# Optimization experiments

Measured on AMD Instinct MI355X. Metric: run time of the kernel, lower is better.

The kernel has to match this reference:

```python
import jax, jax.numpy as jnp
import numpy as np
import math

VOCAB = 50257
BLOCK = 2048
NE = 768


def setup_inputs() -> dict:
    key = jax.random.key(0)
    ks = jax.random.split(key, 12)
    s = 0.02
    idx = jax.random.randint(ks[0], (4, 2048), 0, VOCAB, dtype=jnp.int64 if jax.config.jax_enable_x64 else jnp.int32)
    tok_emb = jax.random.normal(ks[1], (VOCAB, NE), jnp.float32) * s
    pos_emb = jax.random.normal(ks[2], (BLOCK, NE), jnp.float32) * s
    Wk = jax.random.normal(ks[3], (NE, NE), jnp.float32) * s
    bk = jnp.zeros((NE,), jnp.float32)
    Wq = jax.random.normal(ks[4], (NE, NE), jnp.float32) * s
    bq = jnp.zeros((NE,), jnp.float32)
    Wv = jax.random.normal(ks[5], (NE, NE), jnp.float32) * s
    bv = jnp.zeros((NE,), jnp.float32)
    ln_g = jnp.ones((NE,), jnp.float32)
    ln_b = jnp.zeros((NE,), jnp.float32)
    Wh = jax.random.normal(ks[6], (NE, VOCAB), jnp.float32) * s
    bh = jnp.zeros((VOCAB,), jnp.float32)
    return {"idx": idx, "tok_emb": tok_emb, "pos_emb": pos_emb, "Wq": Wq, "bq": bq,
            "Wk": Wk, "bk": bk, "Wv": Wv, "bv": bv, "ln_g": ln_g, "ln_b": ln_b,
            "Wh": Wh, "bh": bh}


def reference(idx, tok_emb, pos_emb, Wq, bq, Wk, bk, Wv, bv, ln_g, ln_b, Wh, bh):
    B, T = idx.shape
    C = tok_emb.shape[1]
    x = tok_emb[idx] + pos_emb[:T]  # [B,T,C]
    q = jnp.einsum('btc,cd->btd', x, Wq) + bq
    k = jnp.einsum('btc,cd->btd', x, Wk) + bk
    v = jnp.einsum('btc,cd->btd', x, Wv) + bv
    att = jnp.einsum('btd,bsd->bts', q, k) / math.sqrt(C)  # [B,T,T]
    causal = jnp.tril(jnp.ones((T, T), bool))
    att = jnp.where(causal, att, -jnp.inf)
    att = jax.nn.softmax(att, axis=-1)
    y = jnp.einsum('bts,bsd->btd', att, v)
    # LayerNorm (eps=1e-5, torch default)
    mu = jnp.mean(y, axis=-1, keepdims=True)
    var = jnp.mean((y - mu) ** 2, axis=-1, keepdims=True)
    yn = (y - mu) * jax.lax.rsqrt(var + 1e-5) * ln_g + ln_b
    logits = jnp.einsum('btc,cv->btv', yn, Wh) + bh
    return logits
```

## Files before the change

kernel.cpp:

```cpp
#include <hip/hip_runtime.h>
#include <hip/hip_bf16.h>
#include <math.h>

typedef __bf16 bf16x8 __attribute__((ext_vector_type(8)));
typedef float  f32x4  __attribute__((ext_vector_type(4)));

#define GAS(p) ((const __attribute__((address_space(1))) void*)(p))
#define LAS(p) ((__attribute__((address_space(3))) void*)(p))

static constexpr int NE = 768;

__global__ __launch_bounds__(256) void k_embed(const int* __restrict__ idx,
    const float* __restrict__ tok, const float* __restrict__ pos,
    __hip_bfloat16* __restrict__ xb)
{
    int bt = blockIdx.x;
    int t  = bt & 2047;
    int token = idx[bt];
    const float* te = tok + (size_t)token * NE;
    const float* pe = pos + (size_t)t * NE;
    __hip_bfloat16* o = xb + (size_t)bt * NE;
    for (int c = threadIdx.x; c < NE; c += 256)
        o[c] = __float2bfloat16(te[c] + pe[c]);
}

__global__ __launch_bounds__(256) void k_transpose_f32_bf16(
    const float* __restrict__ in, __hip_bfloat16* __restrict__ out,
    int R, int C, int outRows)
{
    __shared__ float tile[32][33];
    int c0 = blockIdx.x * 32, r0 = blockIdx.y * 32;
    int tx = threadIdx.x & 31, ty = threadIdx.x >> 5;
    #pragma unroll
    for (int i = 0; i < 32; i += 8) {
        int r = r0 + ty + i, c = c0 + tx;
        tile[ty + i][tx] = (r < R && c < C) ? in[(size_t)r * C + c] : 0.f;
    }
    __syncthreads();
    #pragma unroll
    for (int i = 0; i < 32; i += 8) {
        int oc = c0 + ty + i, orr = r0 + tx;
        if (oc < outRows && orr < R)
            out[(size_t)oc * R + orr] = __float2bfloat16(tile[tx][ty + i]);
    }
}

__global__ __launch_bounds__(256) void k_transpose_bf16(
    const __hip_bfloat16* __restrict__ in, __hip_bfloat16* __restrict__ out,
    int R, int C)
{
    __shared__ __hip_bfloat16 tile[32][33];
    size_t boff = (size_t)blockIdx.z * R * C;
    int c0 = blockIdx.x * 32, r0 = blockIdx.y * 32;
    int tx = threadIdx.x & 31, ty = threadIdx.x >> 5;
    #pragma unroll
    for (int i = 0; i < 32; i += 8)
        tile[ty + i][tx] = in[boff + (size_t)(r0 + ty + i) * C + (c0 + tx)];
    __syncthreads();
    #pragma unroll
    for (int i = 0; i < 32; i += 8)
        out[boff + (size_t)(c0 + ty + i) * R + (r0 + tx)] = tile[tx][ty + i];
}

__global__ __launch_bounds__(256) void k_pack_bias(const float* __restrict__ bq,
    const float* __restrict__ bk, const float* __restrict__ bv, float* __restrict__ o)
{
    int i = blockIdx.x * 256 + threadIdx.x;
    if (i < 768) o[i] = bq[i];
    else if (i < 1536) o[i] = bk[i - 768];
    else if (i < 2304) o[i] = bv[i - 1536];
}

template<int MODE>
__global__ __launch_bounds__(256) void k_gemm(
    const __hip_bfloat16* __restrict__ A, const __hip_bfloat16* __restrict__ Bt,
    int K, int lda, int ldb,
    size_t strideA, size_t strideB, size_t strideC,
    float* __restrict__ outf, int ldc, int ncols,
    const float* __restrict__ bias, float scale,
    __hip_bfloat16* __restrict__ oq, __hip_bfloat16* __restrict__ ok,
    __hip_bfloat16* __restrict__ ov)
{
    int bn = blockIdx.x, bm = blockIdx.y, bz = blockIdx.z;
    if (MODE == 1 && bn > bm) return;
    __shared__ __align__(16) __hip_bfloat16 As[128 * 32];
    __shared__ __align__(16) __hip_bfloat16 Bs[128 * 32];
    const __hip_bfloat16* Ab = A  + bz * strideA + (size_t)bm * 128 * lda;
    const __hip_bfloat16* Bb = Bt + bz * strideB + (size_t)bn * 128 * ldb;
    int tid = threadIdx.x, w = tid >> 6, lane = tid & 63;
    int wr = w >> 1, wc = w & 1;
    f32x4 acc[4][4] = {};
    int sr = tid >> 2, sc = (tid & 3) * 8;
    int lr = lane & 15, lk = (lane >> 4) * 8;

    for (int k0 = 0; k0 < K; k0 += 32) {
        __syncthreads();
        #pragma unroll
        for (int i = 0; i < 2; ++i) {
            __builtin_amdgcn_global_load_lds(GAS(Ab + (size_t)(i * 64 + sr) * lda + k0 + sc),
                                             LAS((char*)As + i * 4096 + w * 1024), 16, 0, 0);
            __builtin_amdgcn_global_load_lds(GAS(Bb + (size_t)(i * 64 + sr) * ldb + k0 + sc),
                                             LAS((char*)Bs + i * 4096 + w * 1024), 16, 0, 0);
        }
        __syncthreads();
        bf16x8 af[4], bfv[4];
        #pragma unroll
        for (int mi = 0; mi < 4; ++mi)
            af[mi] = *(const bf16x8*)(As + (wr * 64 + mi * 16 + lr) * 32 + lk);
        #pragma unroll
        for (int ni = 0; ni < 4; ++ni)
            bfv[ni] = *(const bf16x8*)(Bs + (wc * 64 + ni * 16 + lr) * 32 + lk);
        #pragma unroll
        for (int mi = 0; mi < 4; ++mi)
            #pragma unroll
            for (int ni = 0; ni < 4; ++ni)
                acc[mi][ni] = __builtin_amdgcn_mfma_f32_16x16x32_bf16(af[mi], bfv[ni], acc[mi][ni], 0, 0, 0);
    }

    int r4 = (lane >> 4) * 4;
    #pragma unroll
    for (int mi = 0; mi < 4; ++mi) {
        #pragma unroll
        for (int ni = 0; ni < 4; ++ni) {
            #pragma unroll
            for (int r = 0; r < 4; ++r) {
                int row = bm * 128 + wr * 64 + mi * 16 + r4 + r;
                int col = bn * 128 + wc * 64 + ni * 16 + lr;
                float v = acc[mi][ni][r];
                if constexpr (MODE == 0) {
                    v += bias[col];
                    __hip_bfloat16 h = __float2bfloat16(v);
                    if (col < 768)       oq[(size_t)row * 768 + col]          = h;
                    else if (col < 1536) ok[(size_t)row * 768 + (col - 768)]  = h;
                    else                 ov[(size_t)row * 768 + (col - 1536)] = h;
                } else if constexpr (MODE == 1) {
                    outf[bz * strideC + (size_t)row * ldc + col] = v * scale;
                } else {
                    outf[bz * strideC + (size_t)row * ldc + col] = v;
                }
            }
        }
    }
}

__global__ __launch_bounds__(512, 2) void k_gemm_head(
    const __hip_bfloat16* __restrict__ A,
    const __hip_bfloat16* __restrict__ Bt,
    float* __restrict__ out, const float* __restrict__ bias, int ldc, int ncols)
{
    constexpr int K = 768, NT = K / 64;
    __shared__ __align__(16) __hip_bfloat16 As[2][256 * 64];
    __shared__ __align__(16) __hip_bfloat16 Bs[2][256 * 64];

    const int bn = blockIdx.x, bm = blockIdx.y;
    const int tid = threadIdx.x;
    const int w = tid >> 6, lane = tid & 63;
    const int wr = w >> 2, wc = w & 3;
    const int lr = lane & 15, lu = lane >> 4;
    const int rswz = lr & 7;

    const int srow = tid >> 3;
    const int sunit = (tid & 7) ^ (srow & 7);
    const size_t Abase = (size_t)bm * 256 * K;
    const size_t Bbase = (size_t)bn * 256 * K;

    auto stageA = [&](int kt, int c, int p) {
        const __hip_bfloat16* src = A + Abase + (size_t)(c * 64 + srow) * K + kt * 64 + sunit * 8;
        __builtin_amdgcn_global_load_lds(GAS(src), LAS(&As[p][c * 4096 + tid * 8]), 16, 0, 0);
    };
    auto stageB = [&](int kt, int c, int p) {
        const __hip_bfloat16* src = Bt + Bbase + (size_t)(c * 64 + srow) * K + kt * 64 + sunit * 8;
        __builtin_amdgcn_global_load_lds(GAS(src), LAS(&Bs[p][c * 4096 + tid * 8]), 16, 0, 0);
    };
    auto rdA = [&](int p, int m, int kk) {
        return *(const bf16x8*)&As[p][(wr * 128 + m * 16 + lr) * 64 + ((kk * 4 + lu) ^ rswz) * 8];
    };
    auto rdB = [&](int p, int n, int kk) {
        return *(const bf16x8*)&Bs[p][(wc * 64 + n * 16 + lr) * 64 + ((kk * 4 + lu) ^ rswz) * 8];
    };

    f32x4 acc[8][4] = {};

    stageB(0, 0, 0); stageB(0, 1, 0); stageB(0, 2, 0); stageB(0, 3, 0);
    stageA(0, 0, 0); stageA(0, 1, 0); stageA(0, 2, 0); stageA(0, 3, 0);
    stageB(1, 0, 1); stageB(1, 1, 1); stageB(1, 2, 1); stageB(1, 3, 1);
    stageA(1, 0, 1); stageA(1, 2, 1);

#define QUAD(Q)                                                                                          \
    {   bf16x8 a00 = rdA(p, 2*(Q),     0), a01 = rdA(p, 2*(Q),     1);                                   \
        bf16x8 a10 = rdA(p, 2*(Q) + 1, 0), a11 = rdA(p, 2*(Q) + 1, 1);                                   \
        __builtin_amdgcn_s_setprio(1);                                                                   \
        _Pragma("unroll")                                                                                \
        for (int n = 0; n < 4; ++n) {                                                                    \
            acc[2*(Q)][n]     = __builtin_amdgcn_mfma_f32_16x16x32_bf16(a00, bf[n][0], acc[2*(Q)][n],     0, 0, 0); \
            acc[2*(Q)][n]     = __builtin_amdgcn_mfma_f32_16x16x32_bf16(a01, bf[n][1], acc[2*(Q)][n],     0, 0, 0); \
            acc[2*(Q) + 1][n] = __builtin_amdgcn_mfma_f32_16x16x32_bf16(a10, bf[n][0], acc[2*(Q) + 1][n], 0, 0, 0); \
            acc[2*(Q) + 1][n] = __builtin_amdgcn_mfma_f32_16x16x32_bf16(a11, bf[n][1], acc[2*(Q) + 1][n], 0, 0, 0); \
        }                                                                                                \
        __builtin_amdgcn_s_setprio(0); }

    for (int kt = 0; kt < NT; ++kt) {
        const int p = kt & 1, pn = p ^ 1;
        if (kt + 1 < NT) {
            stageA(kt + 1, 1, pn); stageA(kt + 1, 3, pn);
            asm volatile("s_waitcnt vmcnt(8)" ::: "memory");
        } else {
            asm volatile("s_waitcnt vmcnt(0)" ::: "memory");
        }
        asm volatile("s_barrier" ::: "memory");
        bf16x8 bf[4][2];
        #pragma unroll
        for (int n = 0; n < 4; ++n) { bf[n][0] = rdB(p, n, 0); bf[n][1] = rdB(p, n, 1); }
        QUAD(0)
        asm volatile("s_barrier" ::: "memory");
        if (kt + 2 < NT) { stageB(kt + 2, 0, p); stageB(kt + 2, 1, p); }
        QUAD(1)
        asm volatile("s_barrier" ::: "memory");
        if (kt + 2 < NT) { stageB(kt + 2, 2, p); stageB(kt + 2, 3, p); }
        QUAD(2)
        asm volatile("s_barrier" ::: "memory");
        if (kt + 2 < NT) { stageA(kt + 2, 0, p); stageA(kt + 2, 2, p); }
        QUAD(3)
        asm volatile("s_barrier" ::: "memory");
    }
#undef QUAD

    const int r4 = lu * 4;
    #pragma unroll
    for (int m = 0; m < 8; ++m) {
        #pragma unroll
        for (int n = 0; n < 4; ++n) {
            int col = bn * 256 + wc * 64 + n * 16 + lr;
            if (col < ncols) {
                float bv_ = bias[col];
                #pragma unroll
                for (int r = 0; r < 4; ++r) {
                    int row = bm * 256 + wr * 128 + m * 16 + r4 + r;
                    out[(size_t)row * ldc + col] = acc[m][n][r] + bv_;
                }
            }
        }
    }
}

__global__ __launch_bounds__(256) void k_softmax(const float* __restrict__ att,
    __hip_bfloat16* __restrict__ P, int T)
{
    int t = blockIdx.x, b = blockIdx.y;
    const float* row = att + ((size_t)b * T + t) * T;
    __hip_bfloat16* prow = P + ((size_t)b * T + t) * T;
    int n = t + 1;
    __shared__ float red[256];
    float mx = -1e30f;
    for (int s = threadIdx.x; s < n; s += 256) mx = fmaxf(mx, row[s]);
    red[threadIdx.x] = mx; __syncthreads();
    for (int o = 128; o > 0; o >>= 1) {
        if (threadIdx.x < o) red[threadIdx.x] = fmaxf(red[threadIdx.x], red[threadIdx.x + o]);
        __syncthreads();
    }
    mx = red[0]; __syncthreads();
    float sum = 0.f;
    for (int s = threadIdx.x; s < n; s += 256) sum += expf(row[s] - mx);
    red[threadIdx.x] = sum; __syncthreads();
    for (int o = 128; o > 0; o >>= 1) {
        if (threadIdx.x < o) red[threadIdx.x] += red[threadIdx.x + o];
        __syncthreads();
    }
    float inv = 1.f / red[0];
    for (int s = threadIdx.x; s < T; s += 256)
        prow[s] = __float2bfloat16(s < n ? expf(row[s] - mx) * inv : 0.f);
}

__global__ __launch_bounds__(256) void k_layernorm(const float* __restrict__ y,
    const float* __restrict__ g, const float* __restrict__ b,
    __hip_bfloat16* __restrict__ yn)
{
    int row = blockIdx.x;
    const float* yr = y + (size_t)row * NE;
    float s = 0.f, s2 = 0.f;
    for (int c = threadIdx.x; c < NE; c += 256) { float v = yr[c]; s += v; s2 += v * v; }
    __shared__ float r1[256], r2[256];
    r1[threadIdx.x] = s; r2[threadIdx.x] = s2; __syncthreads();
    for (int o = 128; o > 0; o >>= 1) {
        if (threadIdx.x < o) { r1[threadIdx.x] += r1[threadIdx.x + o]; r2[threadIdx.x] += r2[threadIdx.x + o]; }
        __syncthreads();
    }
    float mu = r1[0] / NE;
    float var = r2[0] / NE - mu * mu;
    float rs = rsqrtf(var + 1e-5f);
    __hip_bfloat16* o = yn + (size_t)row * NE;
    for (int c = threadIdx.x; c < NE; c += 256)
        o[c] = __float2bfloat16((yr[c] - mu) * rs * g[c] + b[c]);
}

extern "C" void kernel_launch(void* const* d_in, const int* in_sizes, int n_in,
                              void* d_out, int out_size, void* d_ws, size_t ws_size,
                              hipStream_t stream)
{
    const int*   idx  = (const int*)  d_in[0];
    const float* tok  = (const float*)d_in[1];
    const float* pos  = (const float*)d_in[2];
    const float* Wq   = (const float*)d_in[3];
    const float* bq   = (const float*)d_in[4];
    const float* Wk   = (const float*)d_in[5];
    const float* bk   = (const float*)d_in[6];
    const float* Wv   = (const float*)d_in[7];
    const float* bv   = (const float*)d_in[8];
    const float* ln_g = (const float*)d_in[9];
    const float* ln_b = (const float*)d_in[10];
    const float* Wh   = (const float*)d_in[11];
    const float* bh   = (const float*)d_in[12];
    float* out = (float*)d_out;

    const int B = 4, T = 2048, C = 768, V = 50257, Vp = 50432;

    char* p = (char*)d_ws;
    auto take = [&](size_t bytes) { char* r = p; p += (bytes + 255) & ~(size_t)255; return r; };
    __hip_bfloat16* xb    = (__hip_bfloat16*)take((size_t)B * T * C * 2);
    __hip_bfloat16* wqkvT = (__hip_bfloat16*)take((size_t)3 * C * C * 2);
    float*          bqkv  = (float*)take((size_t)3 * C * 4);
    __hip_bfloat16* qb    = (__hip_bfloat16*)take((size_t)B * T * C * 2);
    __hip_bfloat16* kb    = (__hip_bfloat16*)take((size_t)B * T * C * 2);
    __hip_bfloat16* vb    = (__hip_bfloat16*)take((size_t)B * T * C * 2);
    __hip_bfloat16* vT    = (__hip_bfloat16*)take((size_t)B * T * C * 2);
    float*          att   = (float*)take((size_t)B * T * T * 4);
    __hip_bfloat16* P     = (__hip_bfloat16*)take((size_t)B * T * T * 2);
    float*          y     = (float*)take((size_t)B * T * C * 4);
    __hip_bfloat16* yn    = (__hip_bfloat16*)take((size_t)B * T * C * 2);
    __hip_bfloat16* whT   = (__hip_bfloat16*)att;

    float scale = 1.0f / sqrtf((float)C);

    k_embed<<<dim3(B * T), 256, 0, stream>>>(idx, tok, pos, xb);
    k_transpose_f32_bf16<<<dim3(24, 24), 256, 0, stream>>>(Wq, wqkvT,             C, C, C);
    k_transpose_f32_bf16<<<dim3(24, 24), 256, 0, stream>>>(Wk, wqkvT + C * C,     C, C, C);
    k_transpose_f32_bf16<<<dim3(24, 24), 256, 0, stream>>>(Wv, wqkvT + 2 * C * C, C, C, C);
    k_pack_bias<<<dim3(9), 256, 0, stream>>>(bq, bk, bv, bqkv);

    k_gemm<0><<<dim3(18, 64, 1), 256, 0, stream>>>(xb, wqkvT, C, C, C, 0, 0, 0,
        nullptr, 0, 0, bqkv, 1.f, qb, kb, vb);

    k_transpose_bf16<<<dim3(24, 64, B), 256, 0, stream>>>(vb, vT, T, C);

    k_gemm<1><<<dim3(16, 16, B), 256, 0, stream>>>(qb, kb, C, C, C,
        (size_t)T * C, (size_t)T * C, (size_t)T * T, att, T, 0, nullptr, scale,
        nullptr, nullptr, nullptr);

    k_softmax<<<dim3(T, B), 256, 0, stream>>>(att, P, T);

    k_gemm<2><<<dim3(6, 16, B), 256, 0, stream>>>(P, vT, T, T, T,
        (size_t)T * T, (size_t)C * T, (size_t)T * C, y, C, 0, nullptr, 1.f,
        nullptr, nullptr, nullptr);

    k_transpose_f32_bf16<<<dim3(Vp / 32, 24), 256, 0, stream>>>(Wh, whT, C, V, Vp);

    k_layernorm<<<dim3(B * T), 256, 0, stream>>>(y, ln_g, ln_b, yn);

    k_gemm_head<<<dim3(Vp / 256, 32), 512, 0, stream>>>(yn, whT, out, bh, V, V);
}
```

Baseline: 1.367 ms.

## Reschedule head GEMM pipeline by K-half phases and swap grid order for B reuse

Restructures the head GEMM main loop so each k-tile runs in four phases split by M-half and K-half. A fragments are reloaded per phase while B fragments are held across the whole tile, and staging loads are interleaved with explicit waitcnt and sched_barrier fences. The grid is also transposed so consecutive blocks share the same vocab column tile of Wh, which should improve L2 reuse of the large weight matrix. The tighter wait counts and extra barriers risk stalls or races if the vmcnt accounting is off.

```diff
diff --git a/kernel.cpp b/kernel.cpp
--- a/kernel.cpp
+++ b/kernel.cpp
@@ -152,78 +152,110 @@
     __shared__ __align__(16) __hip_bfloat16 As[2][256 * 64];
     __shared__ __align__(16) __hip_bfloat16 Bs[2][256 * 64];
 
-    const int bn = blockIdx.x, bm = blockIdx.y;
+    const int bm = blockIdx.x, bn = blockIdx.y;
     const int tid = threadIdx.x;
     const int w = tid >> 6, lane = tid & 63;
     const int wr = w >> 2, wc = w & 3;
     const int lr = lane & 15, lu = lane >> 4;
-    const int rswz = lr & 7;
-
-    const int srow = tid >> 3;
-    const int sunit = (tid & 7) ^ (srow & 7);
-    const size_t Abase = (size_t)bm * 256 * K;
-    const size_t Bbase = (size_t)bn * 256 * K;
-
-    auto stageA = [&](int kt, int c, int p) {
-        const __hip_bfloat16* src = A + Abase + (size_t)(c * 64 + srow) * K + kt * 64 + sunit * 8;
-        __builtin_amdgcn_global_load_lds(GAS(src), LAS(&As[p][c * 4096 + tid * 8]), 16, 0, 0);
+
+    const int sr = tid >> 3;
+    const int su = (tid & 7) ^ (sr & 7);
+    const __hip_bfloat16* Ab = A  + (size_t)(bm * 256) * K;
+    const __hip_bfloat16* Bb = Bt + (size_t)(bn * 256) * K;
+
+    f32x4 acc[8][4] = {};
+    bf16x8 bq[4][2];
+
+    auto stageA = [&](int kt, int q, int pb) {
+        __builtin_amdgcn_global_load_lds(GAS(Ab + (size_t)(q * 64 + sr) * K + kt * 64 + su * 8),
+                                         LAS(&As[pb][q * 4096 + tid * 8]), 16, 0, 0);
     };
-    auto stageB = [&](int kt, int c, int p) {
-        const __hip_bfloat16* src = Bt + Bbase + (size_t)(c * 64 + srow) * K + kt * 64 + sunit * 8;
-        __builtin_amdgcn_global_load_lds(GAS(src), LAS(&Bs[p][c * 4096 + tid * 8]), 16, 0, 0);
+    auto stageBh = [&](int kt, int h, int pb) {
+        #pragma unroll
+        for (int l = 0; l < 2; ++l) {
+            int vt = l * 512 + tid;
+            int r = vt >> 3, u = (vt & 7) ^ (r & 7);
+            __builtin_amdgcn_global_load_lds(GAS(Bb + (size_t)(h * 128 + r) * K + kt * 64 + u * 8),
+                                             LAS(&Bs[pb][h * 8192 + vt * 8]), 16, 0, 0);
+        }
     };
-    auto rdA = [&](int p, int m, int kk) {
-        return *(const bf16x8*)&As[p][(wr * 128 + m * 16 + lr) * 64 + ((kk * 4 + lu) ^ rswz) * 8];
-    };
-    auto rdB = [&](int p, int n, int kk) {
-        return *(const bf16x8*)&Bs[p][(wc * 64 + n * 16 + lr) * 64 + ((kk * 4 + lu) ^ rswz) * 8];
-    };
-
-    f32x4 acc[8][4] = {};
-
-    stageB(0, 0, 0); stageB(0, 1, 0); stageB(0, 2, 0); stageB(0, 3, 0);
-    stageA(0, 0, 0); stageA(0, 1, 0); stageA(0, 2, 0); stageA(0, 3, 0);
-    stageB(1, 0, 1); stageB(1, 1, 1); stageB(1, 2, 1); stageB(1, 3, 1);
-    stageA(1, 0, 1); stageA(1, 2, 1);
-
-#define QUAD(Q)                                                                                          \
-    {   bf16x8 a00 = rdA(p, 2*(Q),     0), a01 = rdA(p, 2*(Q),     1);                                   \
-        bf16x8 a10 = rdA(p, 2*(Q) + 1, 0), a11 = rdA(p, 2*(Q) + 1, 1);                                   \
-        __builtin_amdgcn_s_setprio(1);                                                                   \
-        _Pragma("unroll")                                                                                \
-        for (int n = 0; n < 4; ++n) {                                                                    \
-            acc[2*(Q)][n]     = __builtin_amdgcn_mfma_f32_16x16x32_bf16(a00, bf[n][0], acc[2*(Q)][n],     0, 0, 0); \
-            acc[2*(Q)][n]     = __builtin_amdgcn_mfma_f32_16x16x32_bf16(a01, bf[n][1], acc[2*(Q)][n],     0, 0, 0); \
-            acc[2*(Q) + 1][n] = __builtin_amdgcn_mfma_f32_16x16x32_bf16(a10, bf[n][0], acc[2*(Q) + 1][n], 0, 0, 0); \
-            acc[2*(Q) + 1][n] = __builtin_amdgcn_mfma_f32_16x16x32_bf16(a11, bf[n][1], acc[2*(Q) + 1][n], 0, 0, 0); \
-        }                                                                                                \
-        __builtin_amdgcn_s_setprio(0); }
+
+#define MFMA_Q(MH, KK)                                                                                     \
+    __builtin_amdgcn_s_setprio(1);                                                                         \
+    _Pragma("unroll")                                                                                      \
+    for (int n = 0; n < 4; ++n) {                                                                          \
+        acc[(MH)*4+0][n] = __builtin_amdgcn_mfma_f32_16x16x32_bf16(af[0], bq[n][KK], acc[(MH)*4+0][n], 0, 0, 0); \
+        acc[(MH)*4+1][n] = __builtin_amdgcn_mfma_f32_16x16x32_bf16(af[1], bq[n][KK], acc[(MH)*4+1][n], 0, 0, 0); \
+        acc[(MH)*4+2][n] = __builtin_amdgcn_mfma_f32_16x16x32_bf16(af[2], bq[n][KK], acc[(MH)*4+2][n], 0, 0, 0); \
+        acc[(MH)*4+3][n] = __builtin_amdgcn_mfma_f32_16x16x32_bf16(af[3], bq[n][KK], acc[(MH)*4+3][n], 0, 0, 0); \
+    }                                                                                                      \
+    __builtin_amdgcn_s_setprio(0);
+
+    stageBh(0, 0, 0); stageBh(0, 1, 0);
+    stageA(0, 0, 0);  stageA(0, 2, 0);
+    stageA(0, 1, 0);  stageA(0, 3, 0);
+    stageBh(1, 0, 1); stageBh(1, 1, 1);
+    stageA(1, 0, 1);  stageA(1, 2, 1);
+    asm volatile("s_waitcnt vmcnt(6)" ::: "memory");
+    asm volatile("s_barrier" ::: "memory");
 
     for (int kt = 0; kt < NT; ++kt) {
         const int p = kt & 1, pn = p ^ 1;
-        if (kt + 1 < NT) {
-            stageA(kt + 1, 1, pn); stageA(kt + 1, 3, pn);
-            asm volatile("s_waitcnt vmcnt(8)" ::: "memory");
-        } else {
-            asm volatile("s_waitcnt vmcnt(0)" ::: "memory");
-        }
-        asm volatile("s_barrier" ::: "memory");
-        bf16x8 bf[4][2];
-        #pragma unroll
-        for (int n = 0; n < 4; ++n) { bf[n][0] = rdB(p, n, 0); bf[n][1] = rdB(p, n, 1); }
-        QUAD(0)
-        asm volatile("s_barrier" ::: "memory");
-        if (kt + 2 < NT) { stageB(kt + 2, 0, p); stageB(kt + 2, 1, p); }
-        QUAD(1)
-        asm volatile("s_barrier" ::: "memory");
-        if (kt + 2 < NT) { stageB(kt + 2, 2, p); stageB(kt + 2, 3, p); }
-        QUAD(2)
-        asm volatile("s_barrier" ::: "memory");
+        bf16x8 af[4];
+        #pragma unroll
+        for (int n = 0; n < 4; ++n) {
+            int row = wc * 64 + n * 16 + lr;
+            bq[n][0] = *(const bf16x8*)&Bs[p][row * 64 + (((0 + lu) ^ (row & 7)) << 3)];
+            bq[n][1] = *(const bf16x8*)&Bs[p][row * 64 + (((4 + lu) ^ (row & 7)) << 3)];
+        }
+        #pragma unroll
+        for (int i = 0; i < 4; ++i) {
+            int row = wr * 128 + i * 16 + lr;
+            af[i] = *(const bf16x8*)&As[p][row * 64 + (((0 + lu) ^ (row & 7)) << 3)];
+        }
+        if (kt + 1 < NT) { stageA(kt + 1, 1, pn); stageA(kt + 1, 3, pn); }
+        asm volatile("s_barrier" ::: "memory");
+        asm volatile("s_waitcnt lgkmcnt(0)" ::: "memory");
+        __builtin_amdgcn_sched_barrier(0);
+        MFMA_Q(0, 0)
+        asm volatile("s_barrier" ::: "memory");
+        #pragma unroll
+        for (int i = 0; i < 4; ++i) {
+            int row = wr * 128 + i * 16 + lr;
+            af[i] = *(const bf16x8*)&As[p][row * 64 + (((4 + lu) ^ (row & 7)) << 3)];
+        }
+        if (kt + 2 < NT) stageBh(kt + 2, 0, p);
+        asm volatile("s_waitcnt vmcnt(8)" ::: "memory");
+        asm volatile("s_barrier" ::: "memory");
+        asm volatile("s_waitcnt lgkmcnt(0)" ::: "memory");
+        __builtin_amdgcn_sched_barrier(0);
+        MFMA_Q(0, 1)
+        asm volatile("s_barrier" ::: "memory");
+        #pragma unroll
+        for (int i = 0; i < 4; ++i) {
+            int row = wr * 128 + 64 + i * 16 + lr;
+            af[i] = *(const bf16x8*)&As[p][row * 64 + (((0 + lu) ^ (row & 7)) << 3)];
+        }
+        if (kt + 2 < NT) stageBh(kt + 2, 1, p);
+        asm volatile("s_barrier" ::: "memory");
+        asm volatile("s_waitcnt lgkmcnt(0)" ::: "memory");
+        __builtin_amdgcn_sched_barrier(0);
+        MFMA_Q(1, 0)
+        asm volatile("s_barrier" ::: "memory");
+        #pragma unroll
+        for (int i = 0; i < 4; ++i) {
+            int row = wr * 128 + 64 + i * 16 + lr;
+            af[i] = *(const bf16x8*)&As[p][row * 64 + (((4 + lu) ^ (row & 7)) << 3)];
+        }
         if (kt + 2 < NT) { stageA(kt + 2, 0, p); stageA(kt + 2, 2, p); }
-        QUAD(3)
-        asm volatile("s_barrier" ::: "memory");
-    }
-#undef QUAD
+        asm volatile("s_waitcnt vmcnt(8)" ::: "memory");
+        asm volatile("s_barrier" ::: "memory");
+        asm volatile("s_waitcnt lgkmcnt(0)" ::: "memory");
+        __builtin_amdgcn_sched_barrier(0);
+        MFMA_Q(1, 1)
+        asm volatile("s_barrier" ::: "memory");
+    }
+#undef MFMA_Q
 
     const int r4 = lu * 4;
     #pragma unroll
@@ -356,5 +388,5 @@
 
     k_layernorm<<<dim3(B * T), 256, 0, stream>>>(y, ln_g, ln_b, yn);
 
-    k_gemm_head<<<dim3(Vp / 256, 32), 512, 0, stream>>>(yn, whT, out, bh, V, V);
-}
+    k_gemm_head<<<dim3(32, Vp / 256), 512, 0, stream>>>(yn, whT, out, bh, V, V);
+}
```

After: 1.552 ms. +13.6%, slower.
